# Optimization experiments

Hardware: AMD Instinct MI355X
Metric: run time of the kernel (lower is better)

## Reference

```python
import jax, jax.numpy as jnp
import numpy as np

B, C, T_C, T_S = 8, 512, 8192, 2048
EPS = 1e-5


def conv1x1(w, b, x):
    # w: [Cout, Cin], b: [Cout], x: [B, Cin, T] -> [B, Cout, T]
    return jnp.einsum('oc,bct->bot', w, x) + b[None, :, None]


def setup_inputs() -> dict:
    key = jax.random.key(0)
    ks = jax.random.split(key, 10)
    s = 1.0 / np.sqrt(C)
    return {
        'content': jax.random.normal(ks[0], (B, C, T_C), jnp.float32),
        'style': jax.random.normal(ks[1], (B, C, T_S), jnp.float32),
        'content_key': jax.random.normal(ks[2], (B, C, T_C), jnp.float32),
        'style_key': jax.random.normal(ks[3], (B, C, T_S), jnp.float32),
        'Wf': jax.random.uniform(ks[4], (C, C), jnp.float32, -s, s),
        'bf': jnp.zeros((C,), jnp.float32),
        'Wg': jax.random.uniform(ks[5], (C, C), jnp.float32, -s, s),
        'bg': jnp.zeros((C,), jnp.float32),
        'Wh': jax.random.uniform(ks[6], (C, C), jnp.float32, -s, s),
        'bh': jnp.zeros((C,), jnp.float32),
    }


def reference(content, style, content_key, style_key, Wf, bf, Wg, bg, Wh, bh):
    F = conv1x1(Wf, bf, content_key)          # [B, C, Tc]
    G = conv1x1(Wg, bg, style_key)            # [B, C, Ts]
    H = conv1x1(Wh, bh, style)                # [B, C, Ts]

    # attention scores over style positions (Ts <= max_sample: no subsampling)
    S = jax.nn.softmax(jnp.einsum('bct,bcs->bts', F, G), axis=-1)  # [B, Tc, Ts]

    style_flat = H.transpose(0, 2, 1)                                # [B, Ts, C]
    mean = jnp.einsum('bts,bsc->btc', S, style_flat)                 # [B, Tc, C]
    second = jnp.einsum('bts,bsc->btc', S, style_flat ** 2)
    std = jnp.sqrt(jax.nn.relu(second - mean ** 2))

    mean = mean.transpose(0, 2, 1)  # [B, C, Tc]
    std = std.transpose(0, 2, 1)

    # mean-variance norm of content per (B, C) over spatial dim, unbiased var
    c_mean = content.mean(axis=-1, keepdims=True)
    c_var = content.var(axis=-1, ddof=1, keepdims=True) + EPS
    normed = (content - c_mean) / jnp.sqrt(c_var)

    return std * normed + mean
```

## Files before the change

kernel.cpp:

```cpp
#include <hip/hip_runtime.h>
#include <hip/hip_fp16.h>


#define B_ 8
#define C_ 512
#define TC 8192
#define TS 2048

typedef unsigned short u16;
typedef __attribute__((ext_vector_type(8))) _Float16 f16x8;
typedef __attribute__((ext_vector_type(4))) float f32x4;

__device__ __forceinline__ u16 f2h(float f) {
  return __half_as_ushort(__float2half(f));
}

__device__ __forceinline__ f32x4 mfma16(f16x8 a, f16x8 b, f32x4 c) {
  return __builtin_amdgcn_mfma_f32_16x16x32_f16(a, b, c, 0, 0, 0);
}

__device__ __forceinline__ void stage16(const u16* g, u16* l) {
  __builtin_amdgcn_global_load_lds(
      (__attribute__((address_space(1))) void*)(const void*)g,
      (__attribute__((address_space(3))) void*)l, 16, 0, 0);
}

#define BARSYNC()                                         \
  do {                                                    \
    asm volatile("s_waitcnt lgkmcnt(0)" ::: "memory");    \
    __builtin_amdgcn_s_barrier();                         \
    __builtin_amdgcn_sched_barrier(0);                    \
  } while (0)

__global__ __launch_bounds__(256) void k_content_stats(
    const float* __restrict__ x, float* __restrict__ cmean, float* __restrict__ crstd) {
  const int row = blockIdx.x;
  const float4* p = (const float4*)(x + (size_t)row * TC);
  float s = 0.f, ss = 0.f;
  for (int i = threadIdx.x; i < TC / 4; i += 256) {
    float4 v = p[i];
    s += v.x + v.y + v.z + v.w;
    ss += v.x * v.x + v.y * v.y + v.z * v.z + v.w * v.w;
  }
#pragma unroll
  for (int d = 1; d < 64; d <<= 1) {
    s += __shfl_xor(s, d);
    ss += __shfl_xor(ss, d);
  }
  __shared__ float rs[4], rss[4];
  if ((threadIdx.x & 63) == 0) {
    rs[threadIdx.x >> 6] = s;
    rss[threadIdx.x >> 6] = ss;
  }
  __syncthreads();
  if (threadIdx.x == 0) {
    float S = rs[0] + rs[1] + rs[2] + rs[3];
    float SS = rss[0] + rss[1] + rss[2] + rss[3];
    float mean = S / (float)TC;
    float var = (SS - S * mean) / (float)(TC - 1);
    cmean[row] = mean;
    crstd[row] = rsqrtf(var + 1e-5f);
  }
}

template <bool TRANS_OUT>
__global__ __launch_bounds__(256, 3) void k_conv(
    const float* __restrict__ X, const float* __restrict__ W,
    const float* __restrict__ bias, u16* __restrict__ Y, int M) {
  const int b = blockIdx.z;
  const int m0 = blockIdx.x * 64;
  const int n0 = blockIdx.y * 256;
  const int tid = threadIdx.x;
  const int w = tid >> 6, ln = tid & 63, lg = ln >> 4, l15 = ln & 15;
  __shared__ u16 As[64][72];
  __shared__ u16 Bs[256][72];
  const float* Xb = X + (size_t)b * C_ * M;
  const f32x4 vzero = {0.f, 0.f, 0.f, 0.f};
  f32x4 acc[4][4];
#pragma unroll
  for (int i = 0; i < 4; ++i)
#pragma unroll
    for (int j = 0; j < 4; ++j) acc[i][j] = vzero;

  const int mq = tid & 15, kq = tid >> 4;
  for (int k0 = 0; k0 < 512; k0 += 64) {
    __syncthreads();
    {
      const float* src = Xb + (size_t)(k0 + kq * 4) * M + m0 + mq * 4;
      float4 r0 = *(const float4*)(src);
      float4 r1 = *(const float4*)(src + M);
      float4 r2 = *(const float4*)(src + 2 * M);
      float4 r3 = *(const float4*)(src + 3 * M);
      *(ushort4*)&As[mq * 4 + 0][kq * 4] =
          make_ushort4(f2h(r0.x), f2h(r1.x), f2h(r2.x), f2h(r3.x));
      *(ushort4*)&As[mq * 4 + 1][kq * 4] =
          make_ushort4(f2h(r0.y), f2h(r1.y), f2h(r2.y), f2h(r3.y));
      *(ushort4*)&As[mq * 4 + 2][kq * 4] =
          make_ushort4(f2h(r0.z), f2h(r1.z), f2h(r2.z), f2h(r3.z));
      *(ushort4*)&As[mq * 4 + 3][kq * 4] =
          make_ushort4(f2h(r0.w), f2h(r1.w), f2h(r2.w), f2h(r3.w));
    }
    {
      const float* src = W + (size_t)(n0 + tid) * 512 + k0;
#pragma unroll
      for (int i = 0; i < 16; ++i) {
        float4 v = *(const float4*)(src + i * 4);
        ushort4 hq = make_ushort4(f2h(v.x), f2h(v.y), f2h(v.z), f2h(v.w));
        *(ushort4*)&Bs[tid][i * 4] = hq;
      }
    }
    __syncthreads();
#pragma unroll
    for (int ks = 0; ks < 2; ++ks) {
      f16x8 a[4], bb[4];
#pragma unroll
      for (int mt = 0; mt < 4; ++mt)
        a[mt] = *(const f16x8*)&As[mt * 16 + l15][ks * 32 + lg * 8];
#pragma unroll
      for (int nt = 0; nt < 4; ++nt)
        bb[nt] = *(const f16x8*)&Bs[w * 64 + nt * 16 + l15][ks * 32 + lg * 8];
#pragma unroll
      for (int mt = 0; mt < 4; ++mt)
#pragma unroll
        for (int nt = 0; nt < 4; ++nt)
          acc[mt][nt] = mfma16(a[mt], bb[nt], acc[mt][nt]);
    }
  }
#pragma unroll
  for (int nt = 0; nt < 4; ++nt) {
    const int n = n0 + w * 64 + nt * 16 + l15;
    const float bv = bias[n];
#pragma unroll
    for (int mt = 0; mt < 4; ++mt) {
      const int mb = m0 + mt * 16 + lg * 4;
      f32x4 v = acc[mt][nt];
      if (!TRANS_OUT) {
        u16* yp = Y + (size_t)b * M * 512 + (size_t)mb * 512 + n;
        yp[0 * 512] = f2h(v[0] + bv);
        yp[1 * 512] = f2h(v[1] + bv);
        yp[2 * 512] = f2h(v[2] + bv);
        yp[3 * 512] = f2h(v[3] + bv);
      } else {
        ushort4 hq = make_ushort4(f2h(v[0] + bv), f2h(v[1] + bv),
                                  f2h(v[2] + bv), f2h(v[3] + bv));
        *(ushort4*)(Y + (size_t)b * 512 * M + (size_t)n * M + mb) = hq;
      }
    }
  }
}

__global__ __launch_bounds__(512, 2) void k_attn(
    const u16* __restrict__ Ft, const u16* __restrict__ Gt,
    const u16* __restrict__ Hm, const float* __restrict__ content,
    const float* __restrict__ cmean, const float* __restrict__ crstd,
    float* __restrict__ out) {
  __shared__ u16 Fq[64 * 512];
  __shared__ u16 UG[2][128 * 64];
  __shared__ u16 UH[2][256 * 32];
  __shared__ u16 Ps[64 * 128];
  __shared__ float red[64][20];
  __shared__ float fin_fac[64];
  __shared__ float fin_invl[64];
  __shared__ float flagv[2];

  const int bid = blockIdx.x;
  const int swz = (bid & 7) * 128 + (bid >> 3);
  const int b = swz >> 7;
  const int t0 = (swz & 127) * 64;
  const int tid = threadIdx.x;
  const int w = tid >> 6, ln = tid & 63, lg = ln >> 4, l15 = ln & 15;

  const u16* Ftb = Ft + ((size_t)b * TC + t0) * C_;
  const u16* Gtb = Gt + (size_t)b * TS * C_;
  const u16* Hb = Hm + (size_t)b * C_ * TS;

  {
    const int r = tid >> 3, c0 = tid & 7;
    const u16* src = Ftb + (size_t)r * C_;
#pragma unroll
    for (int i = 0; i < 8; ++i) {
      const int j = c0 + 8 * i;
      uint4 v = *(const uint4*)(src + j * 8);
      const int sw = (j & 56) | ((j ^ r) & 7);
      *(uint4*)&Fq[r * 512 + sw * 8] = v;
    }
  }
  if (tid < 2) flagv[tid] = 0.f;
  __syncthreads();

  const int cF = lg ^ (l15 & 7);
  const char* pF0 = (const char*)Fq + l15 * 1024 + cF * 16;
  const char* pF1 = (const char*)Fq + l15 * 1024 + (cF ^ 4) * 16;
  const char* pG0 = (const char*)UG + (w * 16 + l15) * 128 + cF * 16;
  const char* pG1 = (const char*)UG + (w * 16 + l15) * 128 + (cF ^ 4) * 16;
  const int cH = lg ^ (l15 & 3) ^ ((l15 >> 2) & 3);
  const char* pH = (const char*)UH + (w * 32 + l15) * 64 + cH * 16;
  const char* pP0 = (const char*)Ps + l15 * 256 + cF * 16;
  const char* pP1 = (const char*)Ps + l15 * 256 + (cF ^ 4) * 16;
  const int cW = ((((w & 3) << 1) | (lg >> 1)) ^ (l15 & 7));
  char* pPw = (char*)Ps + l15 * 256 + (w & 4) * 32 + cW * 16 + (lg & 1) * 8;

  auto readF = [&](int tt, int kc_, int ks) -> f16x8 {
    return *(const f16x8*)((ks ? pF1 : pF0) + tt * 16384 + kc_ * 128);
  };
  auto readG = [&](int bf, int ks) -> f16x8 {
    return *(const f16x8*)((ks ? pG1 : pG0) + bf * 16384);
  };
  auto readH = [&](int bf, int nt) -> f16x8 {
    return *(const f16x8*)(pH + bf * 16384 + nt * 1024);
  };
  auto readPa = [&](int mt, int ksl) -> f16x8 {
    return *(const f16x8*)(((ksl & 1) ? pP1 : pP0) + mt * 4096 + (ksl & 2) * 64);
  };

  const int gl = (ln & 7) ^ ((ln >> 3) & 7);
  const u16* sG[2][2];
#pragma unroll
  for (int sh = 0; sh < 2; ++sh)
#pragma unroll
    for (int i = 0; i < 2; ++i)
      sG[sh][i] = Gtb + (size_t)(sh * 128 + w * 16 + i * 8 + (ln >> 3)) * 512 + gl * 8;
  const int hl = (ln & 3) ^ ((ln >> 2) & 3) ^ ((ln >> 4) & 3);
  const u16* sH[2][2];
#pragma unroll
  for (int ch = 0; ch < 2; ++ch)
#pragma unroll
    for (int i = 0; i < 2; ++i)
      sH[ch][i] = Hb + (size_t)(ch * 256 + w * 32 + i * 16 + (ln >> 2)) * 2048 + hl * 8;

  auto stageG2 = [&](int kc_, int sh, int bf) {
    stage16(sG[sh][0] + kc_ * 64, (u16*)((char*)UG + bf * 16384 + (w * 16 + 0) * 128));
    stage16(sG[sh][1] + kc_ * 64, (u16*)((char*)UG + bf * 16384 + (w * 16 + 8) * 128));
  };
  auto stageH2 = [&](int hc, int bf) {
    const int ch = hc & 1, kslg = hc >> 1;
    stage16(sH[ch][0] + kslg * 32, (u16*)((char*)UH + bf * 16384 + (w * 32 + 0) * 64));
    stage16(sH[ch][1] + kslg * 32, (u16*)((char*)UH + bf * 16384 + (w * 32 + 16) * 64));
  };
  auto stageGn = [&](int sh, int bf, int dnext) {
    stage16(sG[sh][0] + dnext, (u16*)((char*)UG + bf * 16384 + (w * 16 + 0) * 128));
    stage16(sG[sh][1] + dnext, (u16*)((char*)UG + bf * 16384 + (w * 16 + 8) * 128));
  };

  stageG2(0, 0, 0);
  stageG2(0, 1, 1);

  const f32x4 vzero = {0.f, 0.f, 0.f, 0.f};
  f32x4 pvm[4][2][2], pvs[4][2][2];
#pragma unroll
  for (int mt = 0; mt < 4; ++mt)
#pragma unroll
    for (int ch = 0; ch < 2; ++ch)
#pragma unroll
      for (int nt = 0; nt < 2; ++nt) {
        pvm[mt][ch][nt] = vzero;
        pvs[mt][ch][nt] = vzero;
      }
  float m_run[4] = {-1e30f, -1e30f, -1e30f, -1e30f};
  float l_run[4] = {0.f, 0.f, 0.f, 0.f};
  const float LOG2E = 1.44269504f;

  for (int st = 0; st < 8; ++st) {
    if (st > 0) {
#pragma unroll
      for (int sh = 0; sh < 2; ++sh)
#pragma unroll
        for (int i = 0; i < 2; ++i) {
          sG[sh][i] += 131072;
          sH[sh][i] += 256;
        }
    }
    const int dnext = (st == 7) ? -917504 : 131072;
    f32x4 sacc[2][4];
#pragma unroll
    for (int sh = 0; sh < 2; ++sh)
#pragma unroll
      for (int tt = 0; tt < 4; ++tt) sacc[sh][tt] = vzero;

#pragma unroll
    for (int kc = 0; kc < 8; ++kc) {
      f16x8 fA[2][4];
#pragma unroll
      for (int sh = 0; sh < 2; ++sh) {
        const int q = kc * 2 + sh;
        asm volatile("s_waitcnt vmcnt(2)" ::: "memory");
        const int bf = q & 1;
        if (sh == 0) {
#pragma unroll
          for (int ks = 0; ks < 2; ++ks)
#pragma unroll
            for (int tt = 0; tt < 4; ++tt) fA[ks][tt] = readF(tt, kc, ks);
        }
        __builtin_amdgcn_s_setprio(1);
#pragma unroll
        for (int ks = 0; ks < 2; ++ks) {
          f16x8 gv = readG(bf, ks);
          sacc[sh][0] = mfma16(gv, fA[ks][0], sacc[sh][0]);
          sacc[sh][1] = mfma16(gv, fA[ks][1], sacc[sh][1]);
          sacc[sh][2] = mfma16(gv, fA[ks][2], sacc[sh][2]);
          sacc[sh][3] = mfma16(gv, fA[ks][3], sacc[sh][3]);
        }
        __builtin_amdgcn_s_setprio(0);
        const int qn = q + 2;
        if (qn < 16) stageG2(qn >> 1, qn & 1, bf);
        else stageH2(qn - 16, bf);
      }
    }

    float mx4[4];
#pragma unroll
    for (int tt = 0; tt < 4; ++tt) {
      f32x4 v0 = sacc[0][tt] * LOG2E;
      f32x4 v1 = sacc[1][tt] * LOG2E;
      float mx = fmaxf(fmaxf(fmaxf(v0[0], v0[1]), fmaxf(v0[2], v0[3])),
                       fmaxf(fmaxf(v1[0], v1[1]), fmaxf(v1[2], v1[3])));
      mx = fmaxf(mx, __shfl_xor(mx, 16));
      mx = fmaxf(mx, __shfl_xor(mx, 32));
      f32x4 p0, p1;
#pragma unroll
      for (int rg = 0; rg < 4; ++rg) {
        p0[rg] = exp2f(v0[rg] - mx);
        p1[rg] = exp2f(v1[rg] - mx);
      }
      float sm = p0[0] + p0[1] + p0[2] + p0[3] + p1[0] + p1[1] + p1[2] + p1[3];
      sm += __shfl_xor(sm, 16);
      sm += __shfl_xor(sm, 32);
      sacc[0][tt] = p0;
      sacc[1][tt] = p1;
      mx4[tt] = mx;
      if (lg == 0)
        *(float2*)&red[tt * 16 + l15][w * 2] = make_float2(mx, sm);
    }
    BARSYNC();

    float fac_p[4];
    {
      bool changed = false;
#pragma unroll
      for (int tt = 0; tt < 4; ++tt) {
        const int row = tt * 16 + l15;
        float4 r0 = *(const float4*)&red[row][0];
        float4 r1 = *(const float4*)&red[row][4];
        float4 r2 = *(const float4*)&red[row][8];
        float4 r3 = *(const float4*)&red[row][12];
        float mc = fmaxf(m_run[tt],
                   fmaxf(fmaxf(fmaxf(r0.x, r0.z), fmaxf(r1.x, r1.z)),
                         fmaxf(fmaxf(r2.x, r2.z), fmaxf(r3.x, r3.z))));
        const float m_new = (mc - m_run[tt] <= 11.0f) ? m_run[tt] : mc;
        float l_new = l_run[tt] * exp2f(m_run[tt] - m_new);
        l_new += r0.y * exp2f(r0.x - m_new) + r0.w * exp2f(r0.z - m_new);
        l_new += r1.y * exp2f(r1.x - m_new) + r1.w * exp2f(r1.z - m_new);
        l_new += r2.y * exp2f(r2.x - m_new) + r2.w * exp2f(r2.z - m_new);
        l_new += r3.y * exp2f(r3.x - m_new) + r3.w * exp2f(r3.z - m_new);
        fac_p[tt] = exp2f(mx4[tt] - m_new);
        if (m_new != m_run[tt]) changed = true;
        if (w == 0 && lg == 0) {
          fin_fac[row] = exp2f(m_run[tt] - m_new);
          if (st == 7) fin_invl[row] = 1.0f / l_new;
        }
        m_run[tt] = m_new;
        l_run[tt] = l_new;
      }
      if (w == 0 && changed) flagv[st & 1] = 1.0f;
    }
#pragma unroll
    for (int tt = 0; tt < 4; ++tt) {
      const f32x4 pe = sacc[0][tt];
      const float fp = fac_p[tt];
      ushort4 pk = make_ushort4(f2h(pe[0] * fp), f2h(pe[1] * fp),
                                f2h(pe[2] * fp), f2h(pe[3] * fp));
      *(ushort4*)(pPw + tt * 4096) = pk;
    }
    BARSYNC();

    {
      const float fl = flagv[st & 1];
      if (fl != 0.f) {
#pragma unroll
        for (int mt = 0; mt < 4; ++mt) {
          const f32x4 fac = *(const f32x4*)&fin_fac[mt * 16 + lg * 4];
#pragma unroll
          for (int ch = 0; ch < 2; ++ch)
#pragma unroll
            for (int nt = 0; nt < 2; ++nt) {
              pvm[mt][ch][nt] *= fac;
              pvs[mt][ch][nt] *= fac;
            }
        }
      }
      if (tid == 0) flagv[(st + 1) & 1] = 0.f;
    }

#pragma unroll
    for (int half = 0; half < 2; ++half) {
      if (half == 1) {
        BARSYNC();
#pragma unroll
        for (int tt = 0; tt < 4; ++tt) {
          const f32x4 pe = sacc[1][tt];
          const float fp = fac_p[tt];
          ushort4 pk = make_ushort4(f2h(pe[0] * fp), f2h(pe[1] * fp),
                                    f2h(pe[2] * fp), f2h(pe[3] * fp));
          *(ushort4*)(pPw + tt * 4096) = pk;
        }
        BARSYNC();
      }
      f16x8 pf0, pf1, pf2, pf3;
#pragma unroll
      for (int pp = 0; pp < 8; ++pp) {
        const int P_ = half * 8 + pp;
        asm volatile("s_waitcnt vmcnt(2)" ::: "memory");
        const int bf = P_ & 1;
        const int ch = pp & 1, ksl = pp >> 1;
        if (ch == 0) {
          pf0 = readPa(0, ksl);
          pf1 = readPa(1, ksl);
          pf2 = readPa(2, ksl);
          pf3 = readPa(3, ksl);
        }
        f16x8 h0 = readH(bf, 0), h1 = readH(bf, 1);
        f16x8 q0 = h0 * h0, q1 = h1 * h1;
        __builtin_amdgcn_s_setprio(1);
        pvm[0][ch][0] = mfma16(pf0, h0, pvm[0][ch][0]);
        pvm[1][ch][0] = mfma16(pf1, h0, pvm[1][ch][0]);
        pvm[2][ch][0] = mfma16(pf2, h0, pvm[2][ch][0]);
        pvm[3][ch][0] = mfma16(pf3, h0, pvm[3][ch][0]);
        pvs[0][ch][0] = mfma16(pf0, q0, pvs[0][ch][0]);
        pvs[1][ch][0] = mfma16(pf1, q0, pvs[1][ch][0]);
        pvs[2][ch][0] = mfma16(pf2, q0, pvs[2][ch][0]);
        pvs[3][ch][0] = mfma16(pf3, q0, pvs[3][ch][0]);
        pvm[0][ch][1] = mfma16(pf0, h1, pvm[0][ch][1]);
        pvm[1][ch][1] = mfma16(pf1, h1, pvm[1][ch][1]);
        pvm[2][ch][1] = mfma16(pf2, h1, pvm[2][ch][1]);
        pvm[3][ch][1] = mfma16(pf3, h1, pvm[3][ch][1]);
        pvs[0][ch][1] = mfma16(pf0, q1, pvs[0][ch][1]);
        pvs[1][ch][1] = mfma16(pf1, q1, pvs[1][ch][1]);
        pvs[2][ch][1] = mfma16(pf2, q1, pvs[2][ch][1]);
        pvs[3][ch][1] = mfma16(pf3, q1, pvs[3][ch][1]);
        __builtin_amdgcn_s_setprio(0);
        const int pn = P_ + 2;
        if (pn < 16) stageH2(pn, bf);
        else stageGn(pn - 16, bf, dnext);
      }
    }
  }
  asm volatile("s_waitcnt vmcnt(0)" ::: "memory");

  f32x4 invq[4];
#pragma unroll
  for (int mt = 0; mt < 4; ++mt)
    invq[mt] = *(const f32x4*)&fin_invl[mt * 16 + lg * 4];
#pragma unroll
  for (int ch = 0; ch < 2; ++ch)
#pragma unroll
    for (int nt = 0; nt < 2; ++nt) {
      const int c = ch * 256 + w * 32 + nt * 16 + l15;
      const size_t row = (size_t)b * C_ + c;
      const float cm = cmean[row];
      const float cr = crstd[row];
      const float* cp = content + row * TC + t0;
      float* op = out + row * TC + t0;
#pragma unroll
      for (int mt = 0; mt < 4; ++mt) {
        const int q0 = mt * 16 + lg * 4;
        const float4 x = *(const float4*)(cp + q0);
        const f32x4 mu = pvm[mt][ch][nt] * invq[mt];
        const f32x4 se = pvs[mt][ch][nt] * invq[mt];
        float4 y;
        y.x = sqrtf(fmaxf(se[0] - mu[0] * mu[0], 0.f)) * ((x.x - cm) * cr) + mu[0];
        y.y = sqrtf(fmaxf(se[1] - mu[1] * mu[1], 0.f)) * ((x.y - cm) * cr) + mu[1];
        y.z = sqrtf(fmaxf(se[2] - mu[2] * mu[2], 0.f)) * ((x.z - cm) * cr) + mu[2];
        y.w = sqrtf(fmaxf(se[3] - mu[3] * mu[3], 0.f)) * ((x.w - cm) * cr) + mu[3];
        *(float4*)(op + q0) = y;
      }
    }
}

extern "C" void kernel_launch(void* const* d_in, const int* in_sizes, int n_in,
                              void* d_out, int out_size, void* d_ws, size_t ws_size,
                              hipStream_t stream) {
  (void)in_sizes;
  (void)n_in;
  (void)out_size;
  (void)ws_size;
  const float* content = (const float*)d_in[0];
  const float* style = (const float*)d_in[1];
  const float* content_key = (const float*)d_in[2];
  const float* style_key = (const float*)d_in[3];
  const float* Wf = (const float*)d_in[4];
  const float* bf = (const float*)d_in[5];
  const float* Wg = (const float*)d_in[6];
  const float* bg = (const float*)d_in[7];
  const float* Wh = (const float*)d_in[8];
  const float* bh = (const float*)d_in[9];
  float* out = (float*)d_out;

  char* ws = (char*)d_ws;
  u16* Ft = (u16*)(ws);
  u16* Gt = (u16*)(ws + 67108864);
  u16* Hm = (u16*)(ws + 83886080);
  float* cmean = (float*)(ws + 100663296);
  float* crstd = (float*)(ws + 100663296 + 16384);

  k_content_stats<<<dim3(B_ * C_), dim3(256), 0, stream>>>(content, cmean, crstd);
  k_conv<false><<<dim3(TC / 64, 2, B_), dim3(256), 0, stream>>>(content_key, Wf, bf, Ft, TC);
  k_conv<false><<<dim3(TS / 64, 2, B_), dim3(256), 0, stream>>>(style_key, Wg, bg, Gt, TS);
  k_conv<true><<<dim3(TS / 64, 2, B_), dim3(256), 0, stream>>>(style, Wh, bh, Hm, TS);

  k_attn<<<dim3(1024), dim3(512), 0, stream>>>(Ft, Gt, Hm, content, cmean, crstd, out);
}
```

Before: 770.9 us.

## Fold Wf into style-key projection and read raw content_key in attention

```diff
diff --git a/kernel.cpp b/kernel.cpp
--- a/kernel.cpp
+++ b/kernel.cpp
@@ -61,6 +61,115 @@
     cmean[row] = mean;
     crstd[row] = rsqrtf(var + 1e-5f);
   }
+}
+
+__global__ __launch_bounds__(256) void k_wfg(
+    const float* __restrict__ Wf, const float* __restrict__ Wg,
+    float* __restrict__ Wfg) {
+  const int i0 = blockIdx.x * 64;
+  const int j0 = blockIdx.y * 256;
+  const int tid = threadIdx.x;
+  const int w = tid >> 6, ln = tid & 63, lg = ln >> 4, l15 = ln & 15;
+  __shared__ u16 As[64][72];
+  __shared__ u16 Bs[256][72];
+  const f32x4 vzero = {0.f, 0.f, 0.f, 0.f};
+  f32x4 acc[4][4];
+#pragma unroll
+  for (int i = 0; i < 4; ++i)
+#pragma unroll
+    for (int j = 0; j < 4; ++j) acc[i][j] = vzero;
+
+  for (int o0 = 0; o0 < 512; o0 += 64) {
+    __syncthreads();
+    {
+      const int iq = tid & 15, oq = tid >> 4;
+      const float* src = Wf + (size_t)(o0 + oq * 4) * 512 + i0 + iq * 4;
+      float4 r0 = *(const float4*)(src);
+      float4 r1 = *(const float4*)(src + 512);
+      float4 r2 = *(const float4*)(src + 1024);
+      float4 r3 = *(const float4*)(src + 1536);
+      *(ushort4*)&As[iq * 4 + 0][oq * 4] = make_ushort4(f2h(r0.x), f2h(r1.x), f2h(r2.x), f2h(r3.x));
+      *(ushort4*)&As[iq * 4 + 1][oq * 4] = make_ushort4(f2h(r0.y), f2h(r1.y), f2h(r2.y), f2h(r3.y));
+      *(ushort4*)&As[iq * 4 + 2][oq * 4] = make_ushort4(f2h(r0.z), f2h(r1.z), f2h(r2.z), f2h(r3.z));
+      *(ushort4*)&As[iq * 4 + 3][oq * 4] = make_ushort4(f2h(r0.w), f2h(r1.w), f2h(r2.w), f2h(r3.w));
+    }
+    {
+      const int jq = tid & 63, og = tid >> 6;
+#pragma unroll
+      for (int ii = 0; ii < 4; ++ii) {
+        const int oq = og * 4 + ii;
+        const float* src = Wg + (size_t)(o0 + oq * 4) * 512 + j0 + jq * 4;
+        float4 r0 = *(const float4*)(src);
+        float4 r1 = *(const float4*)(src + 512);
+        float4 r2 = *(const float4*)(src + 1024);
+        float4 r3 = *(const float4*)(src + 1536);
+        *(ushort4*)&Bs[jq * 4 + 0][oq * 4] = make_ushort4(f2h(r0.x), f2h(r1.x), f2h(r2.x), f2h(r3.x));
+        *(ushort4*)&Bs[jq * 4 + 1][oq * 4] = make_ushort4(f2h(r0.y), f2h(r1.y), f2h(r2.y), f2h(r3.y));
+        *(ushort4*)&Bs[jq * 4 + 2][oq * 4] = make_ushort4(f2h(r0.z), f2h(r1.z), f2h(r2.z), f2h(r3.z));
+        *(ushort4*)&Bs[jq * 4 + 3][oq * 4] = make_ushort4(f2h(r0.w), f2h(r1.w), f2h(r2.w), f2h(r3.w));
+      }
+    }
+    __syncthreads();
+#pragma unroll
+    for (int ks = 0; ks < 2; ++ks) {
+      f16x8 a[4], bb[4];
+#pragma unroll
+      for (int mt = 0; mt < 4; ++mt)
+        a[mt] = *(const f16x8*)&As[mt * 16 + l15][ks * 32 + lg * 8];
+#pragma unroll
+      for (int nt = 0; nt < 4; ++nt)
+        bb[nt] = *(const f16x8*)&Bs[w * 64 + nt * 16 + l15][ks * 32 + lg * 8];
+#pragma unroll
+      for (int mt = 0; mt < 4; ++mt)
+#pragma unroll
+        for (int nt = 0; nt < 4; ++nt)
+          acc[mt][nt] = mfma16(a[mt], bb[nt], acc[mt][nt]);
+    }
+  }
+#pragma unroll
+  for (int nt = 0; nt < 4; ++nt) {
+    const int n = j0 + w * 64 + nt * 16 + l15;
+#pragma unroll
+    for (int mt = 0; mt < 4; ++mt) {
+      const int mb = i0 + mt * 16 + lg * 4;
+      f32x4 v = acc[mt][nt];
+      float* yp = Wfg + (size_t)mb * 512 + n;
+      yp[0 * 512] = v[0];
+      yp[1 * 512] = v[1];
+      yp[2 * 512] = v[2];
+      yp[3 * 512] = v[3];
+    }
+  }
+}
+
+__global__ __launch_bounds__(512) void k_wbeta(
+    const float* __restrict__ Wf, const float* __restrict__ Wg,
+    const float* __restrict__ bfv, const float* __restrict__ bgv,
+    float* __restrict__ wb, float* __restrict__ bp, float* __restrict__ c0) {
+  const int j = threadIdx.x;
+  float a = 0.f, b2 = 0.f;
+  for (int o = 0; o < 512; ++o) {
+    a += bfv[o] * Wg[(size_t)o * 512 + j];
+    b2 += bgv[o] * Wf[(size_t)o * 512 + j];
+  }
+  wb[j] = a;
+  bp[j] = b2;
+  if (j == 0) {
+    float c = 0.f;
+    for (int o = 0; o < 512; ++o) c += bfv[o] * bgv[o];
+    *c0 = c;
+  }
+}
+
+__global__ __launch_bounds__(256) void k_beta(
+    const float* __restrict__ sk, const float* __restrict__ wb,
+    const float* __restrict__ c0, float* __restrict__ beta) {
+  const int b = blockIdx.y;
+  const int s = blockIdx.x * 256 + threadIdx.x;
+  const float* p = sk + (size_t)b * 512 * TS + s;
+  float acc = *c0;
+  for (int j = 0; j < 512; ++j) acc += wb[j] * p[(size_t)j * TS];
+  beta[b * TS + s] = acc;
 }
 
 template <bool TRANS_OUT>
@@ -150,10 +259,10 @@
 }
 
 __global__ __launch_bounds__(512, 2) void k_attn(
-    const u16* __restrict__ Ft, const u16* __restrict__ Gt,
-    const u16* __restrict__ Hm, const float* __restrict__ content,
-    const float* __restrict__ cmean, const float* __restrict__ crstd,
-    float* __restrict__ out) {
+    const float* __restrict__ ck, const u16* __restrict__ Gt,
+    const u16* __restrict__ Hm, const float* __restrict__ betap,
+    const float* __restrict__ content, const float* __restrict__ cmean,
+    const float* __restrict__ crstd, float* __restrict__ out) {
   __shared__ u16 Fq[64 * 512];
   __shared__ u16 UG[2][128 * 64];
   __shared__ u16 UH[2][256 * 32];
@@ -170,19 +279,33 @@
   const int tid = threadIdx.x;
   const int w = tid >> 6, ln = tid & 63, lg = ln >> 4, l15 = ln & 15;
 
-  const u16* Ftb = Ft + ((size_t)b * TC + t0) * C_;
   const u16* Gtb = Gt + (size_t)b * TS * C_;
   const u16* Hb = Hm + (size_t)b * C_ * TS;
 
   {
-    const int r = tid >> 3, c0 = tid & 7;
-    const u16* src = Ftb + (size_t)r * C_;
-#pragma unroll
-    for (int i = 0; i < 8; ++i) {
-      const int j = c0 + 8 * i;
-      uint4 v = *(const uint4*)(src + j * 8);
-      const int sw = (j & 56) | ((j ^ r) & 7);
-      *(uint4*)&Fq[r * 512 + sw * 8] = v;
+    const int tq = tid & 15;
+    const int jq0 = (tid >> 4) * 4;
+    const float* ckb = ck + (size_t)b * C_ * TC + t0;
+#pragma unroll
+    for (int i = 0; i < 4; ++i) {
+      const int jq = jq0 + i;
+      const float* src = ckb + (size_t)(jq * 4) * TC + tq * 4;
+      float4 r0 = *(const float4*)(src);
+      float4 r1 = *(const float4*)(src + TC);
+      float4 r2 = *(const float4*)(src + 2 * TC);
+      float4 r3 = *(const float4*)(src + 3 * TC);
+      const int g = jq >> 1, half = (jq & 1) * 8;
+      const float* q0 = (const float*)&r0;
+      const float* q1 = (const float*)&r1;
+      const float* q2 = (const float*)&r2;
+      const float* q3 = (const float*)&r3;
+#pragma unroll
+      for (int dt = 0; dt < 4; ++dt) {
+        const int t = tq * 4 + dt;
+        const int sw = (g & 56) | ((g ^ t) & 7);
+        ushort4 pk = make_ushort4(f2h(q0[dt]), f2h(q1[dt]), f2h(q2[dt]), f2h(q3[dt]));
+        *(ushort4*)((char*)Fq + t * 1024 + sw * 16 + half) = pk;
+      }
     }
   }
   if (tid < 2) flagv[tid] = 0.f;
@@ -259,6 +382,7 @@
   float m_run[4] = {-1e30f, -1e30f, -1e30f, -1e30f};
   float l_run[4] = {0.f, 0.f, 0.f, 0.f};
   const float LOG2E = 1.44269504f;
+  const float* betab = betap + b * TS + w * 16 + lg * 4;
 
   for (int st = 0; st < 8; ++st) {
     if (st > 0) {
@@ -304,6 +428,18 @@
         const int qn = q + 2;
         if (qn < 16) stageG2(qn >> 1, qn & 1, bf);
         else stageH2(qn - 16, bf);
+      }
+    }
+
+    {
+      const float4 be0 = *(const float4*)(betab + st * 256);
+      const float4 be1 = *(const float4*)(betab + st * 256 + 128);
+      f32x4 bv0 = {be0.x, be0.y, be0.z, be0.w};
+      f32x4 bv1 = {be1.x, be1.y, be1.z, be1.w};
+#pragma unroll
+      for (int tt = 0; tt < 4; ++tt) {
+        sacc[0][tt] += bv0;
+        sacc[1][tt] += bv1;
       }
     }
 
@@ -496,16 +632,23 @@
   float* out = (float*)d_out;
 
   char* ws = (char*)d_ws;
-  u16* Ft = (u16*)(ws);
+  float* Wfg = (float*)(ws);
+  float* wbeta = (float*)(ws + 1048576);
+  float* bprime = (float*)(ws + 1048576 + 4096);
+  float* c0p = (float*)(ws + 1048576 + 8192);
+  float* beta = (float*)(ws + 1048576 + 12288);
   u16* Gt = (u16*)(ws + 67108864);
   u16* Hm = (u16*)(ws + 83886080);
   float* cmean = (float*)(ws + 100663296);
   float* crstd = (float*)(ws + 100663296 + 16384);
 
   k_content_stats<<<dim3(B_ * C_), dim3(256), 0, stream>>>(content, cmean, crstd);
-  k_conv<false><<<dim3(TC / 64, 2, B_), dim3(256), 0, stream>>>(content_key, Wf, bf, Ft, TC);
-  k_conv<false><<<dim3(TS / 64, 2, B_), dim3(256), 0, stream>>>(style_key, Wg, bg, Gt, TS);
+  k_wfg<<<dim3(8, 2), dim3(256), 0, stream>>>(Wf, Wg, Wfg);
+  k_wbeta<<<dim3(1), dim3(512), 0, stream>>>(Wf, Wg, bf, bg, wbeta, bprime, c0p);
+  k_beta<<<dim3(8, 8), dim3(256), 0, stream>>>(style_key, wbeta, c0p, beta);
+  k_conv<false><<<dim3(TS / 64, 2, B_), dim3(256), 0, stream>>>(style_key, Wfg, bprime, Gt, TS);
   k_conv<true><<<dim3(TS / 64, 2, B_), dim3(256), 0, stream>>>(style, Wh, bh, Hm, TS);
 
-  k_attn<<<dim3(1024), dim3(512), 0, stream>>>(Ft, Gt, Hm, content, cmean, crstd, out);
-}
+  k_attn<<<dim3(1024), dim3(512), 0, stream>>>(content_key, Gt, Hm, beta, content,
+                                               cmean, crstd, out);
+}
```

Measured after the change: 731.8 us. 5.1% less time.
